# Optimization experiments

Hardware: AMD Instinct MI355X
Metric: run time of the kernel (lower is better)

The kernel has to match this reference:

```python
import jax, jax.numpy as jnp
import numpy as np

ALPHA = 0.2  # leakyrelu negative slope

def setup_inputs() -> dict:
    key = jax.random.key(0)
    k1, k2, k3 = jax.random.split(key, 3)
    N, F_in, F_out = 8192, 512, 256
    input_x = jax.random.normal(k1, (N, F_in), dtype=jnp.float32)
    # xavier-ish scaling for params
    W = jax.random.normal(k2, (F_in, F_out), dtype=jnp.float32) * (1.414 * (2.0 / (F_in + F_out)) ** 0.5)
    a = jax.random.normal(k3, (2 * F_out, 1), dtype=jnp.float32) * (1.414 * (2.0 / (2 * F_out + 1)) ** 0.5)
    return {"input_x": input_x, "W": W, "a": a}

def reference(input_x, W, a):
    # h: [N, F_out]
    h = input_x @ W
    F_out = W.shape[1]
    # e_ij = leakyrelu([h_i || h_j] @ a) = leakyrelu(h_i @ a1 + h_j @ a2)
    s1 = h @ a[:F_out, 0]   # [N] contribution of row node i
    s2 = h @ a[F_out:, 0]   # [N] contribution of col node j
    e = jax.nn.leaky_relu(s1[:, None] + s2[None, :], negative_slope=ALPHA)  # [N, N]
    attention = jax.nn.softmax(e, axis=1)
    # dropout p=0.0 (eval) -> identity
    h_prime = attention @ h  # [N, F_out]
    return jax.nn.elu(h_prime)  # concat=True
```

## Files before the change

### kernel.cpp

```cpp
#include <hip/hip_runtime.h>
#include <hip/hip_bf16.h>

#define N_NODES 8192
#define F_IN    512
#define F_OUT   256
#define ALPHA   0.2f
#define CHUNK   32
#define NCHUNK  (N_NODES / CHUNK)
#define SEG     1024

__global__ __launch_bounds__(256) void gemm_h(const float* __restrict__ A,
                                              const float* __restrict__ B,
                                              float* __restrict__ C) {
    __shared__ float As[16][68];
    __shared__ float Bs[16][68];
    const int t  = threadIdx.x;
    const int m0 = blockIdx.y * 64;
    const int n0 = blockIdx.x * 64;

    const int arow = t >> 2;
    const int ac4  = (t & 3) * 4;
    const int brow = t >> 4;
    const int bc4  = (t & 15) * 4;
    const int ty = t >> 4;
    const int tx = t & 15;

    float acc[4][4] = {};

    for (int k0 = 0; k0 < F_IN; k0 += 16) {
        float4 av = *(const float4*)(A + (size_t)(m0 + arow) * F_IN + k0 + ac4);
        float4 bv = *(const float4*)(B + (size_t)(k0 + brow) * F_OUT + n0 + bc4);
        __syncthreads();
        As[ac4 + 0][arow] = av.x;
        As[ac4 + 1][arow] = av.y;
        As[ac4 + 2][arow] = av.z;
        As[ac4 + 3][arow] = av.w;
        *(float4*)(&Bs[brow][bc4]) = bv;
        __syncthreads();
        #pragma unroll
        for (int k = 0; k < 16; ++k) {
            const float4 a4 = *(const float4*)(&As[k][ty * 4]);
            const float4 b4 = *(const float4*)(&Bs[k][tx * 4]);
            acc[0][0] += a4.x * b4.x; acc[0][1] += a4.x * b4.y;
            acc[0][2] += a4.x * b4.z; acc[0][3] += a4.x * b4.w;
            acc[1][0] += a4.y * b4.x; acc[1][1] += a4.y * b4.y;
            acc[1][2] += a4.y * b4.z; acc[1][3] += a4.y * b4.w;
            acc[2][0] += a4.z * b4.x; acc[2][1] += a4.z * b4.y;
            acc[2][2] += a4.z * b4.z; acc[2][3] += a4.z * b4.w;
            acc[3][0] += a4.w * b4.x; acc[3][1] += a4.w * b4.y;
            acc[3][2] += a4.w * b4.z; acc[3][3] += a4.w * b4.w;
        }
    }
    #pragma unroll
    for (int r = 0; r < 4; ++r) {
        float4 o = make_float4(acc[r][0], acc[r][1], acc[r][2], acc[r][3]);
        *(float4*)(C + (size_t)(m0 + ty * 4 + r) * F_OUT + n0 + tx * 4) = o;
    }
}

__global__ __launch_bounds__(256) void s12_kernel(const float* __restrict__ h,
                                                  const float* __restrict__ a,
                                                  float* __restrict__ s1,
                                                  float* __restrict__ s2) {
    const int wave = threadIdx.x >> 6;
    const int lane = threadIdx.x & 63;
    const int row  = blockIdx.x * 4 + wave;

    const float4 hv = *(const float4*)(h + (size_t)row * F_OUT + lane * 4);
    const float4 a1 = *(const float4*)(a + lane * 4);
    const float4 a2 = *(const float4*)(a + F_OUT + lane * 4);

    float p1 = hv.x * a1.x + hv.y * a1.y + hv.z * a1.z + hv.w * a1.w;
    float p2 = hv.x * a2.x + hv.y * a2.y + hv.z * a2.z + hv.w * a2.w;
    #pragma unroll
    for (int off = 32; off; off >>= 1) {
        p1 += __shfl_xor(p1, off);
        p2 += __shfl_xor(p2, off);
    }
    if (lane == 0) { s1[row] = p1; s2[row] = p2; }
}

__global__ __launch_bounds__(1024) void seg_sort(const float* __restrict__ s2,
                                                 float* __restrict__ v,
                                                 int* __restrict__ p) {
    __shared__ float sv[SEG];
    __shared__ int   sp[SEG];
    const int t    = threadIdx.x;
    const int base = blockIdx.x * SEG;
    sv[t] = s2[base + t];
    sp[t] = base + t;
    __syncthreads();
    for (int k = 2; k <= SEG; k <<= 1) {
        for (int j = k >> 1; j > 0; j >>= 1) {
            const int ixj = t ^ j;
            if (ixj > t) {
                const bool up = ((t & k) == 0);
                const float av = sv[t], bv = sv[ixj];
                if (up ? (av > bv) : (av < bv)) {
                    sv[t] = bv; sv[ixj] = av;
                    const int pa = sp[t]; sp[t] = sp[ixj]; sp[ixj] = pa;
                }
            }
            __syncthreads();
        }
    }
    v[base + t] = sv[t];
    p[base + t] = sp[t];
}

__global__ __launch_bounds__(256) void merge_pass(const float* __restrict__ vin,
                                                  const int* __restrict__ pin,
                                                  float* __restrict__ vout,
                                                  int* __restrict__ pout,
                                                  int L) {
    const int gid   = blockIdx.x * 256 + threadIdx.x;
    const int pair  = gid / (2 * L);
    const int local = gid - pair * 2 * L;
    const int beg   = pair * 2 * L;

    if (local < L) {
        const int i     = local;
        const float key = vin[beg + i];
        const int  idx  = pin[beg + i];
        const float* Brun = vin + beg + L;
        int lo = 0, hi = L;
        while (lo < hi) {
            const int mid = (lo + hi) >> 1;
            if (Brun[mid] < key) lo = mid + 1; else hi = mid;
        }
        vout[beg + i + lo] = key;
        pout[beg + i + lo] = idx;
    } else {
        const int i     = local - L;
        const float key = vin[beg + L + i];
        const int  idx  = pin[beg + L + i];
        const float* Arun = vin + beg;
        int lo = 0, hi = L;
        while (lo < hi) {
            const int mid = (lo + hi) >> 1;
            if (Arun[mid] <= key) lo = mid + 1; else hi = mid;
        }
        vout[beg + lo + i] = key;
        pout[beg + lo + i] = idx;
    }
}

__global__ __launch_bounds__(256) void chunk_sums(const float* __restrict__ h,
                                                  const float* __restrict__ v,
                                                  const int* __restrict__ p,
                                                  float* __restrict__ cneg,
                                                  float* __restrict__ cpos,
                                                  float* __restrict__ czn,
                                                  float* __restrict__ czp) {
    const int c = blockIdx.x;
    const int f = threadIdx.x;
    const float M = v[N_NODES - 1];
    float accN = 0.f, accP = 0.f, zn = 0.f, zp = 0.f;
    #pragma unroll 8
    for (int tt = 0; tt < CHUNK; ++tt) {
        const int j = c * CHUNK + tt;
        const float vj = v[j];
        const int pj   = p[j];
        const float wn = __expf(ALPHA * vj);
        const float wp = __expf(vj - M);
        const float hv = h[(size_t)pj * F_OUT + f];
        accN += wn * hv; accP += wp * hv;
        zn += wn; zp += wp;
    }
    cneg[c * F_OUT + f] = accN;
    cpos[c * F_OUT + f] = accP;
    if (f == 0) { czn[c] = zn; czp[c] = zp; }
}

__global__ __launch_bounds__(256) void scan_chunks(float* __restrict__ cneg,
                                                   float* __restrict__ cpos,
                                                   float* __restrict__ czn,
                                                   float* __restrict__ czp) {
    const int f = threadIdx.x;
    float run = 0.f;
    for (int c = 0; c < NCHUNK; ++c) {
        const float tv = cneg[c * F_OUT + f];
        cneg[c * F_OUT + f] = run;
        run += tv;
    }
    float runp = 0.f;
    for (int c = NCHUNK - 1; c >= 0; --c) {
        const float tv = cpos[c * F_OUT + f];
        cpos[c * F_OUT + f] = runp;
        runp += tv;
    }
    if (f == 0) {
        float r = 0.f;
        for (int c = 0; c < NCHUNK; ++c) { const float tv = czn[c]; czn[c] = r; r += tv; }
        float rp = 0.f;
        for (int c = NCHUNK - 1; c >= 0; --c) { const float tv = czp[c]; czp[c] = rp; rp += tv; }
    }
}

__global__ __launch_bounds__(256) void fill_prefix(const float* __restrict__ h,
                                                   const float* __restrict__ v,
                                                   const int* __restrict__ p,
                                                   const float* __restrict__ cneg,
                                                   const float* __restrict__ cpos,
                                                   const float* __restrict__ czn,
                                                   const float* __restrict__ czp,
                                                   float* __restrict__ prefN,
                                                   float* __restrict__ sufP,
                                                   float* __restrict__ prefZ,
                                                   float* __restrict__ sufZ) {
    const int c = blockIdx.x;
    const int f = threadIdx.x;
    const float M = v[N_NODES - 1];

    float runN = cneg[c * F_OUT + f];
    float zr   = czn[c];
    #pragma unroll 8
    for (int tt = 0; tt < CHUNK; ++tt) {
        const int j = c * CHUNK + tt;
        prefN[(size_t)j * F_OUT + f] = runN;
        if (f == 0) prefZ[j] = zr;
        const float vj = v[j];
        const int pj   = p[j];
        const float wn = __expf(ALPHA * vj);
        runN += wn * h[(size_t)pj * F_OUT + f];
        if (f == 0) zr += wn;
    }
    if (c == NCHUNK - 1) {
        prefN[(size_t)N_NODES * F_OUT + f] = runN;
        sufP[(size_t)N_NODES * F_OUT + f] = 0.f;
        if (f == 0) { prefZ[N_NODES] = zr; sufZ[N_NODES] = 0.f; }
    }

    float runP = cpos[c * F_OUT + f];
    float zpr  = czp[c];
    #pragma unroll 8
    for (int tt = CHUNK - 1; tt >= 0; --tt) {
        const int j = c * CHUNK + tt;
        const float vj = v[j];
        const int pj   = p[j];
        const float wp = __expf(vj - M);
        runP += wp * h[(size_t)pj * F_OUT + f];
        if (f == 0) zpr += wp;
        sufP[(size_t)j * F_OUT + f] = runP;
        if (f == 0) sufZ[j] = zpr;
    }
}

__global__ __launch_bounds__(256) void rows_kernel(const float* __restrict__ s1,
                                                   const float* __restrict__ v,
                                                   const float* __restrict__ prefN,
                                                   const float* __restrict__ sufP,
                                                   const float* __restrict__ prefZ,
                                                   const float* __restrict__ sufZ,
                                                   float* __restrict__ out) {
    const int wave = threadIdx.x >> 6;
    const int lane = threadIdx.x & 63;
    const int i = blockIdx.x * 4 + wave;

    const float s1v = s1[i];
    const float M   = v[N_NODES - 1];

    const float thr = -s1v;
    int lo = 0, hi = N_NODES;
    while (lo < hi) {
        const int mid = (lo + hi) >> 1;
        if (v[mid] < thr) lo = mid + 1; else hi = mid;
    }
    const int k = lo;

    const float x  = s1v + M;
    const float m  = (x >= 0.f) ? x : ALPHA * x;
    const float cp = __expf(x - m);
    const float cn = __expf(ALPHA * s1v - m);

    const float Z    = cp * sufZ[k] + cn * prefZ[k];
    const float invZ = 1.0f / Z;

    const float4 sp4 = *(const float4*)(sufP  + (size_t)k * F_OUT + lane * 4);
    const float4 pn4 = *(const float4*)(prefN + (size_t)k * F_OUT + lane * 4);

    float4 o;
    o.x = (cp * sp4.x + cn * pn4.x) * invZ;
    o.y = (cp * sp4.y + cn * pn4.y) * invZ;
    o.z = (cp * sp4.z + cn * pn4.z) * invZ;
    o.w = (cp * sp4.w + cn * pn4.w) * invZ;
    o.x = (o.x > 0.f) ? o.x : expm1f(o.x);
    o.y = (o.y > 0.f) ? o.y : expm1f(o.y);
    o.z = (o.z > 0.f) ? o.z : expm1f(o.z);
    o.w = (o.w > 0.f) ? o.w : expm1f(o.w);
    *(float4*)(out + (size_t)i * F_OUT + lane * 4) = o;
}

__global__ __launch_bounds__(1024) void maxs2_kernel(const float* __restrict__ s2,
                                                     float* __restrict__ M) {
    __shared__ float red[1024];
    float m = -1e30f;
    for (int i = threadIdx.x; i < N_NODES; i += 1024) m = fmaxf(m, s2[i]);
    red[threadIdx.x] = m;
    __syncthreads();
    for (int s = 512; s; s >>= 1) {
        if (threadIdx.x < s) red[threadIdx.x] = fmaxf(red[threadIdx.x], red[threadIdx.x + s]);
        __syncthreads();
    }
    if (threadIdx.x == 0) M[0] = red[0];
}

__global__ __launch_bounds__(256) void aggregate_kernel(const float* __restrict__ h,
                                                        const float* __restrict__ s1,
                                                        const float* __restrict__ s2,
                                                        const float* __restrict__ Mptr,
                                                        float* __restrict__ out) {
    __shared__ float w_lds[32][33];
    __shared__ float s2t[32];
    __shared__ float s1_loc[32];
    __shared__ float m_loc[32];

    const int t  = threadIdx.x;
    const int i0 = blockIdx.x * 32;
    const float Mv = Mptr[0];

    if (t < 32) {
        const float s1v = s1[i0 + t];
        s1_loc[t] = s1v;
        const float x = s1v + Mv;
        m_loc[t] = (x >= 0.f) ? x : ALPHA * x;
    }
    __syncthreads();

    const int g  = t >> 6;
    const int fl = t & 63;
    const int f4 = fl * 4;

    float acc[8][4] = {};
    float zacc[8]   = {};

    for (int j0 = 0; j0 < N_NODES; j0 += 32) {
        __syncthreads();
        if (t < 32) s2t[t] = s2[j0 + t];
        __syncthreads();
        #pragma unroll
        for (int q = 0; q < 4; ++q) {
            const int idx = t + q * 256;
            const int il  = idx >> 5;
            const int jl  = idx & 31;
            float e = s1_loc[il] + s2t[jl];
            e = (e >= 0.f) ? e : ALPHA * e;
            w_lds[il][jl] = __expf(e - m_loc[il]);
        }
        __syncthreads();

        #pragma unroll 4
        for (int jl = 0; jl < 32; ++jl) {
            const float4 hv = *(const float4*)(h + (size_t)(j0 + jl) * F_OUT + f4);
            #pragma unroll
            for (int r = 0; r < 8; ++r) {
                const float w = w_lds[g * 8 + r][jl];
                acc[r][0] += w * hv.x;
                acc[r][1] += w * hv.y;
                acc[r][2] += w * hv.z;
                acc[r][3] += w * hv.w;
                zacc[r]   += w;
            }
        }
    }

    #pragma unroll
    for (int r = 0; r < 8; ++r) {
        const int i = i0 + g * 8 + r;
        const float inv = 1.0f / zacc[r];
        float4 o;
        o.x = acc[r][0] * inv; o.y = acc[r][1] * inv;
        o.z = acc[r][2] * inv; o.w = acc[r][3] * inv;
        o.x = (o.x > 0.f) ? o.x : expm1f(o.x);
        o.y = (o.y > 0.f) ? o.y : expm1f(o.y);
        o.z = (o.z > 0.f) ? o.z : expm1f(o.z);
        o.w = (o.w > 0.f) ? o.w : expm1f(o.w);
        *(float4*)(out + (size_t)i * F_OUT + f4) = o;
    }
}

extern "C" void kernel_launch(void* const* d_in, const int* in_sizes, int n_in,
                              void* d_out, int out_size, void* d_ws, size_t ws_size,
                              hipStream_t stream) {
    const float* x = (const float*)d_in[0];
    const float* W = (const float*)d_in[1];
    const float* a = (const float*)d_in[2];
    float* out = (float*)d_out;

    constexpr size_t SZ_H    = (size_t)N_NODES * F_OUT * 4;
    constexpr size_t SZ_VEC  = (size_t)N_NODES * 4;
    constexpr size_t SZ_CHNK = (size_t)NCHUNK * F_OUT * 4;
    constexpr size_t SZ_CZ   = (size_t)NCHUNK * 4;
    constexpr size_t SZ_PZ   = ((size_t)(N_NODES + 1) * 4 + 255) & ~255ULL;
    constexpr size_t SZ_PREF = (size_t)(N_NODES + 1) * F_OUT * 4;

    constexpr size_t OFF_H     = 0;
    constexpr size_t OFF_S1    = OFF_H + SZ_H;
    constexpr size_t OFF_S2    = OFF_S1 + SZ_VEC;
    constexpr size_t OFF_V0    = OFF_S2 + SZ_VEC;
    constexpr size_t OFF_P0    = OFF_V0 + SZ_VEC;
    constexpr size_t OFF_V1    = OFF_P0 + SZ_VEC;
    constexpr size_t OFF_P1    = OFF_V1 + SZ_VEC;
    constexpr size_t OFF_CZN   = OFF_P1 + SZ_VEC;
    constexpr size_t OFF_CZP   = OFF_CZN + SZ_CZ;
    constexpr size_t OFF_CNEG  = OFF_CZP + SZ_CZ;
    constexpr size_t OFF_CPOS  = OFF_CNEG + SZ_CHNK;
    constexpr size_t OFF_PREFZ = OFF_CPOS + SZ_CHNK;
    constexpr size_t OFF_SUFZ  = OFF_PREFZ + SZ_PZ;
    constexpr size_t OFF_PREFN = OFF_SUFZ + SZ_PZ;
    constexpr size_t OFF_SUFP  = OFF_PREFN + SZ_PREF;
    constexpr size_t REQUIRED  = OFF_SUFP + SZ_PREF;

    char* ws = (char*)d_ws;
    float* h  = (float*)(ws + OFF_H);
    float* s1 = (float*)(ws + OFF_S1);
    float* s2 = (float*)(ws + OFF_S2);

    gemm_h<<<dim3(F_OUT / 64, N_NODES / 64), 256, 0, stream>>>(x, W, h);
    s12_kernel<<<N_NODES / 4, 256, 0, stream>>>(h, a, s1, s2);

    if (ws_size >= REQUIRED) {
        float* v0    = (float*)(ws + OFF_V0);
        int*   p0    = (int*)(ws + OFF_P0);
        float* v1    = (float*)(ws + OFF_V1);
        int*   p1    = (int*)(ws + OFF_P1);
        float* czn   = (float*)(ws + OFF_CZN);
        float* czp   = (float*)(ws + OFF_CZP);
        float* cneg  = (float*)(ws + OFF_CNEG);
        float* cpos  = (float*)(ws + OFF_CPOS);
        float* prefZ = (float*)(ws + OFF_PREFZ);
        float* sufZ  = (float*)(ws + OFF_SUFZ);
        float* prefN = (float*)(ws + OFF_PREFN);
        float* sufP  = (float*)(ws + OFF_SUFP);

        seg_sort<<<N_NODES / SEG, SEG, 0, stream>>>(s2, v0, p0);
        merge_pass<<<N_NODES / 256, 256, 0, stream>>>(v0, p0, v1, p1, 1024);
        merge_pass<<<N_NODES / 256, 256, 0, stream>>>(v1, p1, v0, p0, 2048);
        merge_pass<<<N_NODES / 256, 256, 0, stream>>>(v0, p0, v1, p1, 4096);

        chunk_sums<<<NCHUNK, 256, 0, stream>>>(h, v1, p1, cneg, cpos, czn, czp);
        scan_chunks<<<1, 256, 0, stream>>>(cneg, cpos, czn, czp);
        fill_prefix<<<NCHUNK, 256, 0, stream>>>(h, v1, p1, cneg, cpos, czn, czp,
                                                prefN, sufP, prefZ, sufZ);
        rows_kernel<<<N_NODES / 4, 256, 0, stream>>>(s1, v1, prefN, sufP,
                                                     prefZ, sufZ, out);
    } else {
        float* M = (float*)(ws + OFF_V0);
        maxs2_kernel<<<1, 1024, 0, stream>>>(s2, M);
        aggregate_kernel<<<N_NODES / 32, 256, 0, stream>>>(h, s1, s2, M, out);
    }
}
```

Baseline: 180.1 us.

## Drop per-node prefix arrays; rows recompute within-chunk partial sums from chunk scans

Removes the fill_prefix kernel, which wrote two full N×F prefix/suffix arrays (about 16 MB) that rows_kernel then read back. Each row instead starts from the exclusive chunk-level scan and accumulates up to 32 gathered h rows of its own chunk, splitting them at the sorted threshold. The single-thread serial scan of chunk normalisers becomes a parallel Hillis-Steele scan in shared memory. This trades a large write/read round trip and one launch for about 32 gathered row reads and exponentials per output row, mostly served from cache.

```diff
diff --git a/kernel.cpp b/kernel.cpp
--- a/kernel.cpp
+++ b/kernel.cpp
@@ -178,81 +178,48 @@
                                                    float* __restrict__ czp) {
     const int f = threadIdx.x;
     float run = 0.f;
+    #pragma unroll 4
     for (int c = 0; c < NCHUNK; ++c) {
         const float tv = cneg[c * F_OUT + f];
         cneg[c * F_OUT + f] = run;
         run += tv;
     }
     float runp = 0.f;
+    #pragma unroll 4
     for (int c = NCHUNK - 1; c >= 0; --c) {
         const float tv = cpos[c * F_OUT + f];
         cpos[c * F_OUT + f] = runp;
         runp += tv;
     }
-    if (f == 0) {
-        float r = 0.f;
-        for (int c = 0; c < NCHUNK; ++c) { const float tv = czn[c]; czn[c] = r; r += tv; }
-        float rp = 0.f;
-        for (int c = NCHUNK - 1; c >= 0; --c) { const float tv = czp[c]; czp[c] = rp; rp += tv; }
-    }
-}
-
-__global__ __launch_bounds__(256) void fill_prefix(const float* __restrict__ h,
-                                                   const float* __restrict__ v,
-                                                   const int* __restrict__ p,
-                                                   const float* __restrict__ cneg,
-                                                   const float* __restrict__ cpos,
-                                                   const float* __restrict__ czn,
-                                                   const float* __restrict__ czp,
-                                                   float* __restrict__ prefN,
-                                                   float* __restrict__ sufP,
-                                                   float* __restrict__ prefZ,
-                                                   float* __restrict__ sufZ) {
-    const int c = blockIdx.x;
-    const int f = threadIdx.x;
-    const float M = v[N_NODES - 1];
-
-    float runN = cneg[c * F_OUT + f];
-    float zr   = czn[c];
-    #pragma unroll 8
-    for (int tt = 0; tt < CHUNK; ++tt) {
-        const int j = c * CHUNK + tt;
-        prefN[(size_t)j * F_OUT + f] = runN;
-        if (f == 0) prefZ[j] = zr;
-        const float vj = v[j];
-        const int pj   = p[j];
-        const float wn = __expf(ALPHA * vj);
-        runN += wn * h[(size_t)pj * F_OUT + f];
-        if (f == 0) zr += wn;
-    }
-    if (c == NCHUNK - 1) {
-        prefN[(size_t)N_NODES * F_OUT + f] = runN;
-        sufP[(size_t)N_NODES * F_OUT + f] = 0.f;
-        if (f == 0) { prefZ[N_NODES] = zr; sufZ[N_NODES] = 0.f; }
-    }
-
-    float runP = cpos[c * F_OUT + f];
-    float zpr  = czp[c];
-    #pragma unroll 8
-    for (int tt = CHUNK - 1; tt >= 0; --tt) {
-        const int j = c * CHUNK + tt;
-        const float vj = v[j];
-        const int pj   = p[j];
-        const float wp = __expf(vj - M);
-        runP += wp * h[(size_t)pj * F_OUT + f];
-        if (f == 0) zpr += wp;
-        sufP[(size_t)j * F_OUT + f] = runP;
-        if (f == 0) sufZ[j] = zpr;
-    }
-}
-
-__global__ __launch_bounds__(256) void rows_kernel(const float* __restrict__ s1,
-                                                   const float* __restrict__ v,
-                                                   const float* __restrict__ prefN,
-                                                   const float* __restrict__ sufP,
-                                                   const float* __restrict__ prefZ,
-                                                   const float* __restrict__ sufZ,
-                                                   float* __restrict__ out) {
+    __shared__ float bufn[NCHUNK];
+    __shared__ float bufp[NCHUNK];
+    const float on = czn[f];
+    const float op = czp[f];
+    bufn[f] = on;
+    bufp[f] = op;
+    __syncthreads();
+    #pragma unroll
+    for (int off = 1; off < NCHUNK; off <<= 1) {
+        const float an = (f >= off) ? bufn[f - off] : 0.f;
+        const float ap = (f + off < NCHUNK) ? bufp[f + off] : 0.f;
+        __syncthreads();
+        bufn[f] += an;
+        bufp[f] += ap;
+        __syncthreads();
+    }
+    czn[f] = bufn[f] - on;
+    czp[f] = bufp[f] - op;
+}
+
+__global__ __launch_bounds__(256) void rows2_kernel(const float* __restrict__ s1,
+                                                    const float* __restrict__ v,
+                                                    const int* __restrict__ p,
+                                                    const float* __restrict__ h,
+                                                    const float* __restrict__ cnegS,
+                                                    const float* __restrict__ cposS,
+                                                    const float* __restrict__ cznS,
+                                                    const float* __restrict__ czpS,
+                                                    float* __restrict__ out) {
     const int wave = threadIdx.x >> 6;
     const int lane = threadIdx.x & 63;
     const int i = blockIdx.x * 4 + wave;
@@ -267,23 +234,45 @@
         if (v[mid] < thr) lo = mid + 1; else hi = mid;
     }
     const int k = lo;
+    const int c = min(k >> 5, NCHUNK - 1);
+    const int start = c * CHUNK;
+
+    const float4 bN = *(const float4*)(cnegS + (size_t)c * F_OUT + lane * 4);
+    const float4 bP = *(const float4*)(cposS + (size_t)c * F_OUT + lane * 4);
+    float aN0 = bN.x, aN1 = bN.y, aN2 = bN.z, aN3 = bN.w;
+    float aP0 = bP.x, aP1 = bP.y, aP2 = bP.z, aP3 = bP.w;
+    float zn = cznS[c];
+    float zp = czpS[c];
+
+    #pragma unroll 8
+    for (int tt = 0; tt < CHUNK; ++tt) {
+        const int j = start + tt;
+        const float vj = v[j];
+        const int pj   = p[j];
+        const float4 hv = *(const float4*)(h + (size_t)pj * F_OUT + lane * 4);
+        if (j < k) {
+            const float wn = __expf(ALPHA * vj);
+            aN0 += wn * hv.x; aN1 += wn * hv.y; aN2 += wn * hv.z; aN3 += wn * hv.w;
+            zn += wn;
+        } else {
+            const float wp = __expf(vj - M);
+            aP0 += wp * hv.x; aP1 += wp * hv.y; aP2 += wp * hv.z; aP3 += wp * hv.w;
+            zp += wp;
+        }
+    }
 
     const float x  = s1v + M;
     const float m  = (x >= 0.f) ? x : ALPHA * x;
     const float cp = __expf(x - m);
     const float cn = __expf(ALPHA * s1v - m);
 
-    const float Z    = cp * sufZ[k] + cn * prefZ[k];
-    const float invZ = 1.0f / Z;
-
-    const float4 sp4 = *(const float4*)(sufP  + (size_t)k * F_OUT + lane * 4);
-    const float4 pn4 = *(const float4*)(prefN + (size_t)k * F_OUT + lane * 4);
+    const float invZ = 1.0f / (cp * zp + cn * zn);
 
     float4 o;
-    o.x = (cp * sp4.x + cn * pn4.x) * invZ;
-    o.y = (cp * sp4.y + cn * pn4.y) * invZ;
-    o.z = (cp * sp4.z + cn * pn4.z) * invZ;
-    o.w = (cp * sp4.w + cn * pn4.w) * invZ;
+    o.x = (cp * aP0 + cn * aN0) * invZ;
+    o.y = (cp * aP1 + cn * aN1) * invZ;
+    o.z = (cp * aP2 + cn * aN2) * invZ;
+    o.w = (cp * aP3 + cn * aN3) * invZ;
     o.x = (o.x > 0.f) ? o.x : expm1f(o.x);
     o.y = (o.y > 0.f) ? o.y : expm1f(o.y);
     o.z = (o.z > 0.f) ? o.z : expm1f(o.z);
@@ -391,8 +380,6 @@
     constexpr size_t SZ_VEC  = (size_t)N_NODES * 4;
     constexpr size_t SZ_CHNK = (size_t)NCHUNK * F_OUT * 4;
     constexpr size_t SZ_CZ   = (size_t)NCHUNK * 4;
-    constexpr size_t SZ_PZ   = ((size_t)(N_NODES + 1) * 4 + 255) & ~255ULL;
-    constexpr size_t SZ_PREF = (size_t)(N_NODES + 1) * F_OUT * 4;
 
     constexpr size_t OFF_H     = 0;
     constexpr size_t OFF_S1    = OFF_H + SZ_H;
@@ -405,11 +392,7 @@
     constexpr size_t OFF_CZP   = OFF_CZN + SZ_CZ;
     constexpr size_t OFF_CNEG  = OFF_CZP + SZ_CZ;
     constexpr size_t OFF_CPOS  = OFF_CNEG + SZ_CHNK;
-    constexpr size_t OFF_PREFZ = OFF_CPOS + SZ_CHNK;
-    constexpr size_t OFF_SUFZ  = OFF_PREFZ + SZ_PZ;
-    constexpr size_t OFF_PREFN = OFF_SUFZ + SZ_PZ;
-    constexpr size_t OFF_SUFP  = OFF_PREFN + SZ_PREF;
-    constexpr size_t REQUIRED  = OFF_SUFP + SZ_PREF;
+    constexpr size_t REQUIRED  = OFF_CPOS + SZ_CHNK;
 
     char* ws = (char*)d_ws;
     float* h  = (float*)(ws + OFF_H);
@@ -428,10 +411,6 @@
         float* czp   = (float*)(ws + OFF_CZP);
         float* cneg  = (float*)(ws + OFF_CNEG);
         float* cpos  = (float*)(ws + OFF_CPOS);
-        float* prefZ = (float*)(ws + OFF_PREFZ);
-        float* sufZ  = (float*)(ws + OFF_SUFZ);
-        float* prefN = (float*)(ws + OFF_PREFN);
-        float* sufP  = (float*)(ws + OFF_SUFP);
 
         seg_sort<<<N_NODES / SEG, SEG, 0, stream>>>(s2, v0, p0);
         merge_pass<<<N_NODES / 256, 256, 0, stream>>>(v0, p0, v1, p1, 1024);
@@ -440,10 +419,8 @@
 
         chunk_sums<<<NCHUNK, 256, 0, stream>>>(h, v1, p1, cneg, cpos, czn, czp);
         scan_chunks<<<1, 256, 0, stream>>>(cneg, cpos, czn, czp);
-        fill_prefix<<<NCHUNK, 256, 0, stream>>>(h, v1, p1, cneg, cpos, czn, czp,
-                                                prefN, sufP, prefZ, sufZ);
-        rows_kernel<<<N_NODES / 4, 256, 0, stream>>>(s1, v1, prefN, sufP,
-                                                     prefZ, sufZ, out);
+        rows2_kernel<<<N_NODES / 4, 256, 0, stream>>>(s1, v1, p1, h,
+                                                      cneg, cpos, czn, czp, out);
     } else {
         float* M = (float*)(ws + OFF_V0);
         maxs2_kernel<<<1, 1024, 0, stream>>>(s2, M);
```

After: 198.1 us. 1.1x slower.
